# Performance work log

Measured on AMD Instinct MI355X. Metric: run time of the kernel, lower is better.

The kernel has to match this reference:

```python
import jax, jax.numpy as jnp
import numpy as np

D_MODEL = 1024
D_INNER = 2048   # expand * d_model
D_STATE = 16
DT_RANK = 64     # ceil(d_model / 16)
D_CONV = 4
L = 2048
EPS = 1e-5


def setup_inputs() -> dict:
    key = jax.random.key(0)
    ks = jax.random.split(key, 8)
    sc = lambda k, shape: jax.random.normal(k, shape, jnp.float32) * 0.02
    A = jnp.tile(jnp.arange(1, D_STATE + 1, dtype=jnp.float32), (D_INNER, 1))
    return {
        "x": jax.random.normal(ks[0], (L, D_MODEL), jnp.float32),
        "W_in": sc(ks[1], (D_MODEL, 2 * D_INNER)),          # in_proj (no bias)
        "W_conv": sc(ks[2], (D_CONV, D_INNER)),             # depthwise conv kernel
        "b_conv": jnp.zeros((D_INNER,), jnp.float32),
        "W_x": sc(ks[3], (D_INNER, DT_RANK + 2 * D_STATE)), # x_proj (no bias)
        "W_dt": sc(ks[4], (DT_RANK, D_INNER)),
        "b_dt": jnp.zeros((D_INNER,), jnp.float32),
        "A_log": jnp.log(A),
        "D": jnp.ones((D_INNER,), jnp.float32),
        "W_out": sc(ks[5], (D_INNER, D_MODEL)),             # out_proj (no bias)
        "ln_scale": jnp.ones((D_MODEL,), jnp.float32),
        "ln_bias": jnp.zeros((D_MODEL,), jnp.float32),
        "drop_key": 0,  # unused: training=False -> DropPath is identity
    }


def reference(x, W_in, W_conv, b_conv, W_x, W_dt, b_dt, A_log, D, W_out,
              ln_scale, ln_bias, drop_key):
    l = x.shape[0]
    # LayerNorm (flax default: mean/var over features)
    mu = jnp.mean(x, axis=-1, keepdims=True)
    var = jnp.mean(jnp.square(x), axis=-1, keepdims=True) - jnp.square(mu)
    xn = (x - mu) * jax.lax.rsqrt(var + EPS) * ln_scale + ln_bias

    # MambaBlock
    xr = xn @ W_in                         # (l, 2*d_inner)
    u, res = xr[:, :D_INNER], xr[:, D_INNER:]

    # causal depthwise conv: pad left d_conv-1, take first l outputs
    up = jnp.pad(u, ((D_CONV - 1, 0), (0, 0)))
    uc = b_conv + sum(up[k:k + l] * W_conv[k] for k in range(D_CONV))
    u2 = jax.nn.silu(uc)                   # (l, d_inner)

    # SSM params (input-dependent)
    x_dbl = u2 @ W_x                       # (l, dt_rank + 2n)
    dt = x_dbl[:, :DT_RANK]
    B = x_dbl[:, DT_RANK:DT_RANK + D_STATE]
    C = x_dbl[:, DT_RANK + D_STATE:]
    delta = jax.nn.softplus(dt @ W_dt + b_dt)   # (l, d_inner)
    A = -jnp.exp(A_log)                         # (d_inner, n)

    dA = jnp.exp(jnp.einsum('ld,dn->ldn', delta, A))   # (l, d_inner, n)
    dBu = jnp.einsum('ld,ln->ldn', delta * u2, B)       # (l, d_inner, n)

    def step(h, inp):
        dA_t, dBu_t, C_t = inp
        h = dA_t * h + dBu_t               # (d_inner, n)
        return h, h @ C_t                  # y_t: (d_inner,)

    h0 = jnp.zeros((D_INNER, D_STATE), dtype=u2.dtype)
    _, ys = jax.lax.scan(step, h0, (dA, dBu, C))
    y = ys + u2 * D                        # (l, d_inner)

    y = y * jax.nn.silu(res)
    out = y @ W_out                        # (l, d_model)
    return out + x                         # residual (DropPath identity in eval)
```

## Files before the change

### kernel.cpp

```cpp
#include <hip/hip_runtime.h>
#include <math.h>

#define L_SEQ 2048
#define DM 1024
#define DI 2048
#define DS 16
#define DTR 64
#define EPS 1e-5f
#define NSEG 32
#define SEGLEN 64
#define NSTATE (DI * DS)

typedef float f32x4 __attribute__((ext_vector_type(4)));
typedef __bf16 bf16x8 __attribute__((ext_vector_type(8)));
typedef _Float16 h16x2 __attribute__((ext_vector_type(2)));

static __device__ __forceinline__ unsigned short f2bf(float f) {
  union { float f; unsigned u; } v; v.f = f;
  unsigned r = v.u + 0x7fffu + ((v.u >> 16) & 1u);
  return (unsigned short)(r >> 16);
}
static __device__ __forceinline__ float bf2f(unsigned short s) {
  union { unsigned u; float f; } v; v.u = ((unsigned)s) << 16;
  return v.f;
}

static __device__ __forceinline__ void gload16(const void* g, void* l) {
  __builtin_amdgcn_global_load_lds(
      (__attribute__((address_space(1))) void*)(unsigned long long)(g),
      (__attribute__((address_space(3))) void*)(unsigned)(unsigned long long)(l),
      16, 0, 0);
}

__global__ __launch_bounds__(256) void ln_kernel(const float* __restrict__ x,
                                                 const float* __restrict__ sc,
                                                 const float* __restrict__ bi,
                                                 unsigned short* __restrict__ xnb) {
  int row = blockIdx.x;
  int t = threadIdx.x;
  float4 xv = ((const float4*)(x + (size_t)row * DM))[t];
  float s  = xv.x + xv.y + xv.z + xv.w;
  float s2 = xv.x*xv.x + xv.y*xv.y + xv.z*xv.z + xv.w*xv.w;
  #pragma unroll
  for (int m = 32; m >= 1; m >>= 1) {
    s  += __shfl_xor(s, m);
    s2 += __shfl_xor(s2, m);
  }
  __shared__ float red[8];
  int wid = t >> 6, lane = t & 63;
  if (lane == 0) { red[wid] = s; red[4 + wid] = s2; }
  __syncthreads();
  s  = red[0] + red[1] + red[2] + red[3];
  s2 = red[4] + red[5] + red[6] + red[7];
  float mu = s * (1.f / DM);
  float var = s2 * (1.f / DM) - mu * mu;
  float rs = rsqrtf(var + EPS);
  float4 sc4 = ((const float4*)sc)[t];
  float4 bi4 = ((const float4*)bi)[t];
  ushort4 ob;
  ob.x = f2bf((xv.x - mu) * rs * sc4.x + bi4.x);
  ob.y = f2bf((xv.y - mu) * rs * sc4.y + bi4.y);
  ob.z = f2bf((xv.z - mu) * rs * sc4.z + bi4.z);
  ob.w = f2bf((xv.w - mu) * rs * sc4.w + bi4.w);
  *(ushort4*)&xnb[(size_t)row * DM + t * 4] = ob;
}

__global__ __launch_bounds__(256) void trans_bf16(
    const float* __restrict__ W, unsigned short* __restrict__ Wt, int K, int N)
{
  __shared__ unsigned short s[64][80];
  int n0 = blockIdx.x * 64, k0 = blockIdx.y * 64;
  int tid = threadIdx.x;
  #pragma unroll
  for (int p = 0; p < 4; ++p) {
    int i = p * 16 + (tid >> 4);
    int j = (tid & 15) * 4;
    float4 w = *(const float4*)&W[(size_t)(k0 + i) * N + n0 + j];
    s[j + 0][i] = f2bf(w.x); s[j + 1][i] = f2bf(w.y);
    s[j + 2][i] = f2bf(w.z); s[j + 3][i] = f2bf(w.w);
  }
  __syncthreads();
  #pragma unroll
  for (int q = 0; q < 2; ++q) {
    int n = q * 32 + (tid >> 3);
    int i8 = (tid & 7) * 8;
    *(int4*)&Wt[(size_t)(n0 + n) * K + k0 + i8] = *(const int4*)&s[n][i8];
  }
}

__global__ __launch_bounds__(256) void transpose_b16(
    const unsigned short* __restrict__ in, unsigned short* __restrict__ out,
    int R, int C)
{
  __shared__ unsigned short s[64][72];
  int c0 = blockIdx.x * 64, r0 = blockIdx.y * 64;
  int tid = threadIdx.x;
  #pragma unroll
  for (int p = 0; p < 2; ++p) {
    int r = p * 32 + (tid >> 3);
    int c = (tid & 7) * 8;
    *(int4*)&s[r][c] = *(const int4*)&in[(size_t)(r0 + r) * C + c0 + c];
  }
  __syncthreads();
  #pragma unroll
  for (int p = 0; p < 2; ++p) {
    int c = p * 32 + (tid >> 3);
    int r = (tid & 7) * 8;
    ushort4 a, b;
    a.x = s[r + 0][c]; a.y = s[r + 1][c]; a.z = s[r + 2][c]; a.w = s[r + 3][c];
    b.x = s[r + 4][c]; b.y = s[r + 5][c]; b.z = s[r + 6][c]; b.w = s[r + 7][c];
    *(ushort4*)&out[(size_t)(c0 + c) * R + r0 + r] = a;
    *(ushort4*)&out[(size_t)(c0 + c) * R + r0 + r + 4] = b;
  }
}

__global__ __launch_bounds__(256) void trans_wx(
    const float* __restrict__ Wx, unsigned short* __restrict__ Wxt)
{
  int i = blockIdx.x * 256 + threadIdx.x;
  int n = i >> 11, k = i & 2047;
  Wxt[i] = (n < 96) ? f2bf(Wx[(size_t)k * 96 + n]) : (unsigned short)0;
}

template<int BM, int BN, int EPI, int OUTB, int SPLITK>
__global__ __launch_bounds__(256) void gemm2(
    const unsigned short* __restrict__ A, int lda,
    const unsigned short* __restrict__ Bt, int ldb,
    void* __restrict__ Cv, int ldc,
    int M, int N, int K,
    const float* __restrict__ bias)
{
  constexpr int WM = BM / 2, WN = BN / 2;
  constexpr int FM = WM / 16, FN = WN / 16;
  __shared__ __align__(16) unsigned short smA[BM * 64];
  __shared__ __align__(16) unsigned short smB[BN * 64];

  int nwg = gridDim.x * gridDim.y;
  int bid = blockIdx.y * gridDim.x + blockIdx.x;
  if ((nwg & 7) == 0) {
    int cpx = nwg >> 3;
    bid = (bid & 7) * cpx + (bid >> 3);
  }
  int bx = bid % gridDim.x;
  int by = bid / gridDim.x;
  int m0 = by * BM, n0 = bx * BN;

  int tid = threadIdx.x;
  int lane = tid & 63, wid = tid >> 6;
  int wm = wid >> 1, wn = wid & 1;

  int kb = blockIdx.z * (K / SPLITK);
  int nt = (K / SPLITK) / 64;

  int rs = lane >> 3;
  int cs = (lane & 7) * 8;

  f32x4 acc[FM][FN];
  #pragma unroll
  for (int m = 0; m < FM; ++m)
    #pragma unroll
    for (int n = 0; n < FN; ++n) acc[m][n] = (f32x4){0.f, 0.f, 0.f, 0.f};

  for (int kt = 0; kt < nt; ++kt) {
    __syncthreads();
    #pragma unroll
    for (int i = 0; i < BM / 32; ++i) {
      int chunk = wid * (BM / 32) + i;
      gload16(A + (size_t)(m0 + chunk * 8 + rs) * lda + kb + kt * 64 + cs,
              (char*)smA + chunk * 1024);
    }
    #pragma unroll
    for (int i = 0; i < BN / 32; ++i) {
      int chunk = wid * (BN / 32) + i;
      gload16(Bt + (size_t)(n0 + chunk * 8 + rs) * ldb + kb + kt * 64 + cs,
              (char*)smB + chunk * 1024);
    }
    __syncthreads();

    #pragma unroll
    for (int kk = 0; kk < 2; ++kk) {
      bf16x8 aF[FM], bF[FN];
      #pragma unroll
      for (int m = 0; m < FM; ++m) {
        int r = wm * WM + m * 16 + (lane & 15);
        aF[m] = *(const bf16x8*)((const char*)smA + r * 128 + kk * 64 + (lane >> 4) * 16);
      }
      #pragma unroll
      for (int n = 0; n < FN; ++n) {
        int r = wn * WN + n * 16 + (lane & 15);
        bF[n] = *(const bf16x8*)((const char*)smB + r * 128 + kk * 64 + (lane >> 4) * 16);
      }
      #pragma unroll
      for (int m = 0; m < FM; ++m)
        #pragma unroll
        for (int n = 0; n < FN; ++n)
          acc[m][n] = __builtin_amdgcn_mfma_f32_16x16x32_bf16(
              aF[m], bF[n], acc[m][n], 0, 0, 0);
    }
  }

  float* Cf = (float*)Cv + (size_t)blockIdx.z * M * ldc;
  unsigned short* Cb = (unsigned short*)Cv;
  int cm = (lane >> 4) * 4, cn = lane & 15;
  #pragma unroll
  for (int m = 0; m < FM; ++m)
    #pragma unroll
    for (int n = 0; n < FN; ++n) {
      int col = n0 + wn * WN + n * 16 + cn;
      #pragma unroll
      for (int r = 0; r < 4; ++r) {
        int row = m0 + wm * WM + m * 16 + cm + r;
        float v = acc[m][n][r];
        if (EPI == 1) {
          float w = v + bias[row];
          v = (w > 20.f) ? w : log1pf(__expf(w));
        }
        if (OUTB) Cb[(size_t)row * ldc + col] = f2bf(v);
        else      Cf[(size_t)row * ldc + col] = v;
      }
    }
}

__global__ __launch_bounds__(256) void xdbl_reduce(
    const float* __restrict__ part, unsigned short* __restrict__ xdbl)
{
  int i = (blockIdx.x * 256 + threadIdx.x) * 4;
  const int SL = 2048 * 128;
  float4 s = *(const float4*)&part[i];
  #pragma unroll
  for (int z = 1; z < 16; ++z) {
    float4 p = *(const float4*)&part[(size_t)z * SL + i];
    s.x += p.x; s.y += p.y; s.z += p.z; s.w += p.w;
  }
  ushort4 ob;
  ob.x = f2bf(s.x); ob.y = f2bf(s.y); ob.z = f2bf(s.z); ob.w = f2bf(s.w);
  *(ushort4*)&xdbl[i] = ob;
}

__global__ __launch_bounds__(256) void out_reduce(
    const float* __restrict__ part, const float* __restrict__ x,
    float* __restrict__ out)
{
  int i = (blockIdx.x * 256 + threadIdx.x) * 4;
  const int SL = 2048 * 1024;
  float4 a = *(const float4*)&part[i];
  float4 b = *(const float4*)&part[SL + i];
  float4 r = *(const float4*)&x[i];
  float4 o;
  o.x = a.x + b.x + r.x; o.y = a.y + b.y + r.y;
  o.z = a.z + b.z + r.z; o.w = a.w + b.w + r.w;
  *(float4*)&out[i] = o;
}

__global__ __launch_bounds__(256) void conv_silu_kernel(
    const unsigned short* __restrict__ xrT,
    const float* __restrict__ Wc, const float* __restrict__ bc,
    unsigned short* __restrict__ u2T)
{
  int d = blockIdx.x;
  int l0 = blockIdx.y * 1024 + threadIdx.x * 4;
  const unsigned short* ur = xrT + (size_t)d * L_SEQ;
  float w0 = Wc[0 * DI + d], w1 = Wc[1 * DI + d];
  float w2 = Wc[2 * DI + d], w3 = Wc[3 * DI + d];
  float b = bc[d];
  ushort4 v0 = *(const ushort4*)&ur[l0];
  ushort4 vm; vm.x = vm.y = vm.z = vm.w = 0;
  if (l0 > 0) vm = *(const ushort4*)&ur[l0 - 4];
  float um3 = bf2f(vm.y), um2 = bf2f(vm.z), um1 = bf2f(vm.w);
  float x0 = bf2f(v0.x), x1 = bf2f(v0.y), x2 = bf2f(v0.z), x3 = bf2f(v0.w);
  float y0 = b + w0 * um3 + w1 * um2 + w2 * um1 + w3 * x0;
  float y1 = b + w0 * um2 + w1 * um1 + w2 * x0  + w3 * x1;
  float y2 = b + w0 * um1 + w1 * x0  + w2 * x1  + w3 * x2;
  float y3 = b + w0 * x0  + w1 * x1  + w2 * x2  + w3 * x3;
  ushort4 ob;
  ob.x = f2bf(y0 / (1.f + __expf(-y0)));
  ob.y = f2bf(y1 / (1.f + __expf(-y1)));
  ob.z = f2bf(y2 / (1.f + __expf(-y2)));
  ob.w = f2bf(y3 / (1.f + __expf(-y3)));
  *(ushort4*)&u2T[(size_t)d * L_SEQ + l0] = ob;
}


__global__ __launch_bounds__(128) void scan_pass1(
    const unsigned short* __restrict__ deltaT, const unsigned short* __restrict__ u2T,
    const unsigned short* __restrict__ xdbl,
    const float* __restrict__ A_log,
    float* __restrict__ hend, float* __restrict__ aprod)
{
  int t = threadIdx.x;
  int ch = t >> 4, n = t & 15;
  int li = (t & 15) * 4;
  int d0 = blockIdx.x * 8, d = d0 + ch;
  int base = blockIdx.y * SEGLEN;

  __shared__ __align__(16) float sdT[8][68], suT[8][68], sBT[16][68];

  float An = -__expf(A_log[d * DS + n]);

  ushort4 rdu = *(const ushort4*)&deltaT[(size_t)d * L_SEQ + base + li];
  ushort4 ru  = *(const ushort4*)&u2T[(size_t)d * L_SEQ + base + li];
  ushort4 rB[2];
  #pragma unroll
  for (int q = 0; q < 2; ++q) {
    int ll = base + (t >> 2) + q * 32;
    rB[q] = *(const ushort4*)&xdbl[(size_t)ll * 128 + 64 + (t & 3) * 4];
  }

  float d0v = bf2f(rdu.x), d1v = bf2f(rdu.y), d2v = bf2f(rdu.z), d3v = bf2f(rdu.w);
  sdT[ch][li + 0] = d0v; sdT[ch][li + 1] = d1v;
  sdT[ch][li + 2] = d2v; sdT[ch][li + 3] = d3v;
  suT[ch][li + 0] = d0v * bf2f(ru.x); suT[ch][li + 1] = d1v * bf2f(ru.y);
  suT[ch][li + 2] = d2v * bf2f(ru.z); suT[ch][li + 3] = d3v * bf2f(ru.w);
  #pragma unroll
  for (int q = 0; q < 2; ++q) {
    int ll = (t >> 2) + q * 32;
    int nb = (t & 3) * 4;
    sBT[nb + 0][ll] = bf2f(rB[q].x); sBT[nb + 1][ll] = bf2f(rB[q].y);
    sBT[nb + 2][ll] = bf2f(rB[q].z); sBT[nb + 3][ll] = bf2f(rB[q].w);
  }
  __syncthreads();

  float h = 0.f, P = 1.f;
  #pragma unroll
  for (int g = 0; g < 64; g += 4) {
    float4 dl4 = *(const float4*)&sdT[ch][g];
    float4 du4 = *(const float4*)&suT[ch][g];
    float4 Bn4 = *(const float4*)&sBT[n][g];
    float dl[4] = {dl4.x, dl4.y, dl4.z, dl4.w};
    float du[4] = {du4.x, du4.y, du4.z, du4.w};
    float Bn[4] = {Bn4.x, Bn4.y, Bn4.z, Bn4.w};
    #pragma unroll
    for (int i = 0; i < 4; ++i) {
      float dA = __expf(dl[i] * An);
      P *= dA;
      h = dA * h + du[i] * Bn[i];
    }
  }
  size_t idx = (size_t)blockIdx.y * NSTATE + d0 * DS + t;
  hend[idx]  = h;
  aprod[idx] = P;
}

__global__ __launch_bounds__(256) void scan_pass2(
    const float* __restrict__ hend, const float* __restrict__ aprod,
    float* __restrict__ h_in)
{
  int i = blockIdx.x * 256 + threadIdx.x;
  float h = 0.f;
  h_in[i] = 0.f;
  for (int s = 0; s < NSEG - 1; ++s) {
    h = aprod[(size_t)s * NSTATE + i] * h + hend[(size_t)s * NSTATE + i];
    h_in[(size_t)(s + 1) * NSTATE + i] = h;
  }
}

__global__ __launch_bounds__(128) void scan_pass3(
    const unsigned short* __restrict__ deltaT, const unsigned short* __restrict__ u2T,
    const unsigned short* __restrict__ resT,
    const unsigned short* __restrict__ xdbl,
    const float* __restrict__ A_log, const float* __restrict__ Dp,
    const float* __restrict__ h_in,
    unsigned short* __restrict__ ybT)
{
  int t = threadIdx.x;
  int ch = t >> 4, n = t & 15;
  int li = (t & 15) * 4;
  int d0 = blockIdx.x * 8, d = d0 + ch;
  int s = blockIdx.y;
  int base = s * SEGLEN;

  __shared__ __align__(16) float sdT[8][68], suT[8][68];
  __shared__ __align__(16) float sBT[16][68], sCT[16][68];
  __shared__ __align__(4) _Float16 svh[32][134];

  float An = -__expf(A_log[d * DS + n]);
  float h = h_in[(size_t)s * NSTATE + d0 * DS + t];

  ushort4 rdu = *(const ushort4*)&deltaT[(size_t)d * L_SEQ + base + li];
  ushort4 ru  = *(const ushort4*)&u2T[(size_t)d * L_SEQ + base + li];
  ushort4 rB[2], rC[2];
  #pragma unroll
  for (int q = 0; q < 2; ++q) {
    int ll = base + (t >> 2) + q * 32;
    int n4 = (t & 3) * 4;
    rB[q] = *(const ushort4*)&xdbl[(size_t)ll * 128 + 64 + n4];
    rC[q] = *(const ushort4*)&xdbl[(size_t)ll * 128 + 80 + n4];
  }

  float d0v = bf2f(rdu.x), d1v = bf2f(rdu.y), d2v = bf2f(rdu.z), d3v = bf2f(rdu.w);
  sdT[ch][li + 0] = d0v; sdT[ch][li + 1] = d1v;
  sdT[ch][li + 2] = d2v; sdT[ch][li + 3] = d3v;
  suT[ch][li + 0] = d0v * bf2f(ru.x); suT[ch][li + 1] = d1v * bf2f(ru.y);
  suT[ch][li + 2] = d2v * bf2f(ru.z); suT[ch][li + 3] = d3v * bf2f(ru.w);
  #pragma unroll
  for (int q = 0; q < 2; ++q) {
    int ll = (t >> 2) + q * 32;
    int nb = (t & 3) * 4;
    sBT[nb + 0][ll] = bf2f(rB[q].x); sBT[nb + 1][ll] = bf2f(rB[q].y);
    sBT[nb + 2][ll] = bf2f(rB[q].z); sBT[nb + 3][ll] = bf2f(rB[q].w);
    sCT[nb + 0][ll] = bf2f(rC[q].x); sCT[nb + 1][ll] = bf2f(rC[q].y);
    sCT[nb + 2][ll] = bf2f(rC[q].z); sCT[nb + 3][ll] = bf2f(rC[q].w);
  }
  __syncthreads();

  #pragma unroll
  for (int half = 0; half < 2; ++half) {
    int g0 = half * 32;
    #pragma unroll
    for (int g = g0; g < g0 + 32; g += 4) {
      float4 dl4 = *(const float4*)&sdT[ch][g];
      float4 du4 = *(const float4*)&suT[ch][g];
      float4 Bn4 = *(const float4*)&sBT[n][g];
      float4 Cn4 = *(const float4*)&sCT[n][g];
      float dl[4] = {dl4.x, dl4.y, dl4.z, dl4.w};
      float du[4] = {du4.x, du4.y, du4.z, du4.w};
      float Bn[4] = {Bn4.x, Bn4.y, Bn4.z, Bn4.w};
      float Cn[4] = {Cn4.x, Cn4.y, Cn4.z, Cn4.w};
      #pragma unroll
      for (int i = 0; i < 4; ++i) {
        float dA = __expf(dl[i] * An);
        h = dA * h + du[i] * Bn[i];
        svh[g - g0 + i][t] = (_Float16)(h * Cn[i]);
      }
    }
    __syncthreads();

    #pragma unroll
    for (int r = 0; r < 2; ++r) {
      int idx = r * 128 + t;
      int ll = idx & 31, c2 = idx >> 5;
      const _Float16* row = &svh[ll][c2 * 16];
      float sum = 0.f;
      #pragma unroll
      for (int k = 0; k < 8; ++k) {
        h16x2 pv = *(const h16x2*)&row[k * 2];
        sum += (float)pv.x + (float)pv.y;
      }
      int dd = d0 + c2;
      int lg = base + g0 + ll;
      float uv = bf2f(u2T[(size_t)dd * L_SEQ + lg]);
      float rv = bf2f(resT[(size_t)dd * L_SEQ + lg]);
      float sig = 1.f / (1.f + __expf(-rv));
      float yv = (sum + uv * Dp[dd]) * rv * sig;
      ybT[(size_t)dd * L_SEQ + lg] = f2bf(yv);
    }
    __syncthreads();
  }
}

extern "C" void kernel_launch(void* const* d_in, const int* in_sizes, int n_in,
                              void* d_out, int out_size, void* d_ws, size_t ws_size,
                              hipStream_t stream)
{
  const float* x      = (const float*)d_in[0];
  const float* W_in   = (const float*)d_in[1];
  const float* W_conv = (const float*)d_in[2];
  const float* b_conv = (const float*)d_in[3];
  const float* W_x    = (const float*)d_in[4];
  const float* W_dt   = (const float*)d_in[5];
  const float* b_dt   = (const float*)d_in[6];
  const float* A_log  = (const float*)d_in[7];
  const float* Dp     = (const float*)d_in[8];
  const float* W_out  = (const float*)d_in[9];
  const float* ln_s   = (const float*)d_in[10];
  const float* ln_b   = (const float*)d_in[11];

  char* ws = (char*)d_ws;
  const size_t MB = 1u << 20;
  unsigned short* xnb    = (unsigned short*)(ws);
  unsigned short* xrT    = (unsigned short*)(ws + 4 * MB);
  unsigned short* u2T    = (unsigned short*)(ws + 20 * MB);
  unsigned short* u2b    = (unsigned short*)(ws + 28 * MB);
  float*          hend   = (float*)(ws + 28 * MB);
  float*          aprod  = (float*)(ws + 32 * MB);
  unsigned short* xdbl   = (unsigned short*)(ws + 36 * MB);
  unsigned short* Wxt    = (unsigned short*)(ws + 36 * MB + 512 * 1024);
  unsigned short* Wdt_t  = (unsigned short*)(ws + 37 * MB);
  unsigned short* deltaTb= (unsigned short*)(ws + 38 * MB);
  unsigned short* Wtin   = (unsigned short*)(ws + 38 * MB);
  float*          part   = (float*)(ws + 46 * MB);
  unsigned short* ybT    = (unsigned short*)(ws + 54 * MB);
  float*          h_in   = (float*)(ws + 62 * MB);
  unsigned short* yb     = (unsigned short*)(ws + 4 * MB);
  unsigned short* Wtout  = xnb;
  const unsigned short* resT = xrT + (size_t)DI * L_SEQ;

  ln_kernel<<<L_SEQ, 256, 0, stream>>>(x, ln_s, ln_b, xnb);

  trans_bf16<<<dim3((2 * DI) / 64, DM / 64), 256, 0, stream>>>(W_in, Wtin, DM, 2 * DI);

  gemm2<64, 128, 0, 1, 1><<<dim3(L_SEQ / 128, (2 * DI) / 64), 256, 0, stream>>>(
      Wtin, DM, xnb, DM, xrT, L_SEQ, 2 * DI, L_SEQ, DM, nullptr);

  conv_silu_kernel<<<dim3(DI, 2), 256, 0, stream>>>(xrT, W_conv, b_conv, u2T);

  transpose_b16<<<dim3(L_SEQ / 64, DI / 64), 256, 0, stream>>>(u2T, u2b, DI, L_SEQ);

  trans_wx<<<(128 * 2048) / 256, 256, 0, stream>>>(W_x, Wxt);

  gemm2<64, 128, 0, 0, 16><<<dim3(1, L_SEQ / 64, 16), 256, 0, stream>>>(
      u2b, DI, Wxt, DI, part, 128, L_SEQ, 128, DI, nullptr);

  xdbl_reduce<<<(L_SEQ * 128) / 1024, 256, 0, stream>>>(part, xdbl);

  trans_bf16<<<dim3(DI / 64, DTR / 64), 256, 0, stream>>>(W_dt, Wdt_t, DTR, DI);

  gemm2<64, 128, 1, 1, 1><<<dim3(L_SEQ / 128, DI / 64), 256, 0, stream>>>(
      Wdt_t, DTR, xdbl, 128, deltaTb, L_SEQ, DI, L_SEQ, DTR, b_dt);

  trans_bf16<<<dim3(DM / 64, DI / 64), 256, 0, stream>>>(W_out, Wtout, DI, DM);

  scan_pass1<<<dim3(DI / 8, NSEG - 1), 128, 0, stream>>>(
      deltaTb, u2T, xdbl, A_log, hend, aprod);

  scan_pass2<<<NSTATE / 256, 256, 0, stream>>>(hend, aprod, h_in);

  scan_pass3<<<dim3(DI / 8, NSEG), 128, 0, stream>>>(
      deltaTb, u2T, resT, xdbl, A_log, Dp, h_in, ybT);

  transpose_b16<<<dim3(L_SEQ / 64, DI / 64), 256, 0, stream>>>(ybT, yb, DI, L_SEQ);

  gemm2<64, 64, 0, 0, 2><<<dim3(DM / 64, L_SEQ / 64, 2), 256, 0, stream>>>(
      yb, DI, Wtout, DI, part, DM, L_SEQ, DM, DI, nullptr);

  out_reduce<<<(L_SEQ * DM) / 1024, 256, 0, stream>>>(part, x, (float*)d_out);
}
```

Before: 181.5 us.

## Fuse conv+SiLU with transpose, replace decay product with exp-sum, retile GEMMs

Merges the depthwise conv+SiLU kernel with the following transpose, so one kernel writes both the channel-major and the row-major bf16 copies through shared memory. That saves a kernel launch and a full read of u2T. In scan pass 1, the running product of per-step decays is replaced by exp(An * sum(delta)), which drops a multiply per step. It also changes the loop-carried dependency and can round differently. The in_proj and out_proj GEMM tile sizes are enlarged, trading fewer blocks for more reuse per block.

New measurement: 183.8 us. Within noise of the previous version (+1.3%).

```diff
diff --git a/kernel.cpp b/kernel.cpp
--- a/kernel.cpp
+++ b/kernel.cpp
@@ -252,32 +252,54 @@
   *(float4*)&out[i] = o;
 }
 
-__global__ __launch_bounds__(256) void conv_silu_kernel(
+__global__ __launch_bounds__(256) void conv_silu_fused(
     const unsigned short* __restrict__ xrT,
     const float* __restrict__ Wc, const float* __restrict__ bc,
-    unsigned short* __restrict__ u2T)
-{
-  int d = blockIdx.x;
-  int l0 = blockIdx.y * 1024 + threadIdx.x * 4;
-  const unsigned short* ur = xrT + (size_t)d * L_SEQ;
+    unsigned short* __restrict__ u2T, unsigned short* __restrict__ u2b)
+{
+  __shared__ unsigned short st[128][68];
+  int d0 = blockIdx.x * 64, l0 = blockIdx.y * 128;
+  int tid = threadIdx.x;
+  int dloc = tid & 63;
+  int lp = (tid >> 6) * 32;
+  int d = d0 + dloc;
+  const unsigned short* ur = xrT + (size_t)d * L_SEQ + l0 + lp;
   float w0 = Wc[0 * DI + d], w1 = Wc[1 * DI + d];
   float w2 = Wc[2 * DI + d], w3 = Wc[3 * DI + d];
   float b = bc[d];
-  ushort4 v0 = *(const ushort4*)&ur[l0];
-  ushort4 vm; vm.x = vm.y = vm.z = vm.w = 0;
-  if (l0 > 0) vm = *(const ushort4*)&ur[l0 - 4];
-  float um3 = bf2f(vm.y), um2 = bf2f(vm.z), um1 = bf2f(vm.w);
-  float x0 = bf2f(v0.x), x1 = bf2f(v0.y), x2 = bf2f(v0.z), x3 = bf2f(v0.w);
-  float y0 = b + w0 * um3 + w1 * um2 + w2 * um1 + w3 * x0;
-  float y1 = b + w0 * um2 + w1 * um1 + w2 * x0  + w3 * x1;
-  float y2 = b + w0 * um1 + w1 * x0  + w2 * x1  + w3 * x2;
-  float y3 = b + w0 * x0  + w1 * x1  + w2 * x2  + w3 * x3;
-  ushort4 ob;
-  ob.x = f2bf(y0 / (1.f + __expf(-y0)));
-  ob.y = f2bf(y1 / (1.f + __expf(-y1)));
-  ob.z = f2bf(y2 / (1.f + __expf(-y2)));
-  ob.w = f2bf(y3 / (1.f + __expf(-y3)));
-  *(ushort4*)&u2T[(size_t)d * L_SEQ + l0] = ob;
+
+  ushort4 vin[8];
+  #pragma unroll
+  for (int j = 0; j < 8; ++j) vin[j] = *(const ushort4*)&ur[j * 4];
+  ushort4 vh; vh.x = vh.y = vh.z = vh.w = 0;
+  if (l0 + lp > 0) vh = *(const ushort4*)&ur[-4];
+  float prev3 = bf2f(vh.y), prev2 = bf2f(vh.z), prev1 = bf2f(vh.w);
+
+  #pragma unroll
+  for (int j = 0; j < 8; ++j) {
+    float xs[4] = {bf2f(vin[j].x), bf2f(vin[j].y), bf2f(vin[j].z), bf2f(vin[j].w)};
+    ushort4 ob;
+    unsigned short* o = (unsigned short*)&ob;
+    #pragma unroll
+    for (int i = 0; i < 4; ++i) {
+      float y = b + w0 * prev3 + w1 * prev2 + w2 * prev1 + w3 * xs[i];
+      prev3 = prev2; prev2 = prev1; prev1 = xs[i];
+      float sig = 1.f / (1.f + __expf(-y));
+      o[i] = f2bf(y * sig);
+    }
+    *(ushort4*)&u2T[(size_t)d * L_SEQ + l0 + lp + j * 4] = ob;
+    st[lp + j * 4 + 0][dloc] = o[0];
+    st[lp + j * 4 + 1][dloc] = o[1];
+    st[lp + j * 4 + 2][dloc] = o[2];
+    st[lp + j * 4 + 3][dloc] = o[3];
+  }
+  __syncthreads();
+  int lr = tid >> 1, hf = (tid & 1) * 32;
+  unsigned short* ob = &u2b[(size_t)(l0 + lr) * DI + d0 + hf];
+  *(int4*)&ob[0]  = *(const int4*)&st[lr][hf + 0];
+  *(int4*)&ob[8]  = *(const int4*)&st[lr][hf + 8];
+  *(int4*)&ob[16] = *(const int4*)&st[lr][hf + 16];
+  *(int4*)&ob[24] = *(const int4*)&st[lr][hf + 24];
 }
 
 
@@ -320,7 +342,7 @@
   }
   __syncthreads();
 
-  float h = 0.f, P = 1.f;
+  float h = 0.f, sdl = 0.f;
   #pragma unroll
   for (int g = 0; g < 64; g += 4) {
     float4 dl4 = *(const float4*)&sdT[ch][g];
@@ -332,13 +354,13 @@
     #pragma unroll
     for (int i = 0; i < 4; ++i) {
       float dA = __expf(dl[i] * An);
-      P *= dA;
+      sdl += dl[i];
       h = dA * h + du[i] * Bn[i];
     }
   }
   size_t idx = (size_t)blockIdx.y * NSTATE + d0 * DS + t;
   hend[idx]  = h;
-  aprod[idx] = P;
+  aprod[idx] = __expf(An * sdl);
 }
 
 __global__ __launch_bounds__(256) void scan_pass2(
@@ -489,12 +511,11 @@
 
   trans_bf16<<<dim3((2 * DI) / 64, DM / 64), 256, 0, stream>>>(W_in, Wtin, DM, 2 * DI);
 
-  gemm2<64, 128, 0, 1, 1><<<dim3(L_SEQ / 128, (2 * DI) / 64), 256, 0, stream>>>(
+  gemm2<128, 128, 0, 1, 1><<<dim3(L_SEQ / 128, (2 * DI) / 128), 256, 0, stream>>>(
       Wtin, DM, xnb, DM, xrT, L_SEQ, 2 * DI, L_SEQ, DM, nullptr);
 
-  conv_silu_kernel<<<dim3(DI, 2), 256, 0, stream>>>(xrT, W_conv, b_conv, u2T);
-
-  transpose_b16<<<dim3(L_SEQ / 64, DI / 64), 256, 0, stream>>>(u2T, u2b, DI, L_SEQ);
+  conv_silu_fused<<<dim3(DI / 64, L_SEQ / 128), 256, 0, stream>>>(
+      xrT, W_conv, b_conv, u2T, u2b);
 
   trans_wx<<<(128 * 2048) / 256, 256, 0, stream>>>(W_x, Wxt);
 
@@ -520,7 +541,7 @@
 
   transpose_b16<<<dim3(L_SEQ / 64, DI / 64), 256, 0, stream>>>(ybT, yb, DI, L_SEQ);
 
-  gemm2<64, 64, 0, 0, 2><<<dim3(DM / 64, L_SEQ / 64, 2), 256, 0, stream>>>(
+  gemm2<64, 128, 0, 0, 2><<<dim3(DM / 128, L_SEQ / 64, 2), 256, 0, stream>>>(
       yb, DI, Wtout, DI, part, DM, L_SEQ, DM, DI, nullptr);
 
   out_reduce<<<(L_SEQ * DM) / 1024, 256, 0, stream>>>(part, x, (float*)d_out);
```
